# Kernel optimization log

Measured on AMD Instinct MI355X. Metric: run time of the kernel, lower is better.

## Reference

```python
import jax, jax.numpy as jnp
import numpy as np

M_SQRT1_2 = 0.7071067811865476
P_DROP = 0.1  # activation_dropout


def setup_inputs() -> dict:
    key = jax.random.key(0)
    k1, k2, k3, k4 = jax.random.split(key, 4)
    N, FFN, EMB = 8192, 4096, 1024
    x = jax.random.normal(k1, (N, FFN), dtype=jnp.float16)
    weight = (jax.random.normal(k2, (EMB, FFN), dtype=jnp.float32) * (1.0 / np.sqrt(FFN))).astype(jnp.float16)
    bias = jax.random.normal(k3, (EMB,), dtype=jnp.float16)
    mask = jax.random.uniform(k4, (N, FFN)) >= P_DROP  # keep mask (bool)
    return {"x": x, "weight": weight, "bias": bias, "mask": mask}


def reference(x, weight, bias, mask):
    # GELU computed in fp32, cast back to fp16 (matches the custom IR)
    xf = x.astype(jnp.float32)
    g = (0.5 * xf * (1.0 + jax.lax.erf(xf * M_SQRT1_2))).astype(jnp.float16)
    # dropout: mask then scale by 1/(1-p) in fp16
    scale = jnp.float16(1.0 / (1.0 - P_DROP))
    h = g * mask.astype(jnp.float16) * scale  # [N, FFN]
    # y[N0, N2] = sum_N1 h[N0, N1] * weight[N2, N1] + bias[N2]
    y = jnp.einsum('nf,ef->ne', h, weight) + bias[None, :]
    return y
```

## Files before the change

### kernel.cpp

```cpp
#include <hip/hip_runtime.h>
#include <stdint.h>

typedef uint32_t u32;
typedef uint16_t u16;

static constexpr int M_DIM = 8192;
static constexpr int N_DIM = 1024;
static constexpr int K_DIM = 4096;

static constexpr size_t H_BYTES  = (size_t)M_DIM * K_DIM * 2;
static constexpr size_t FRAG_U16 = 512;
static constexpr size_t WT_BYTES = 64ull * 128 * FRAG_U16 * 2;
static constexpr size_t WS_NEEDED = H_BYTES + WT_BYTES;

typedef __attribute__((ext_vector_type(8))) _Float16 half8;
typedef __attribute__((ext_vector_type(4))) float f32x4;

__device__ __forceinline__ u32 pack2(float a, float b) {
  union { _Float16 h[2]; u32 u; } p;
  p.h[0] = (_Float16)a;
  p.h[1] = (_Float16)b;
  return p.u;
}

__device__ __forceinline__ float gelu_drop(float x, u32 keep) {
  float ax = fabsf(x);
  float z  = ax * 0.70710678f;
  float t  = __builtin_amdgcn_rcpf(fmaf(0.3275911f, z, 1.0f));
  float poly = fmaf(fmaf(fmaf(fmaf(1.061405429f, t, -1.453152027f),
                              t, 1.421413741f),
                         t, -0.284496736f),
                    t, 0.254829592f) * t;
  float e   = exp2f(z * z * -1.44269504f);
  float erf = fmaf(-poly, e, 1.0f);
  float g   = 0.5f * x * (1.0f + copysignf(erf, x));
  return keep ? g * 1.1111112f : 0.0f;
}

__device__ __forceinline__ void async_cp16(const void* g, void* l) {
  __builtin_amdgcn_global_load_lds((__attribute__((address_space(1))) u32*)g,
                                   (__attribute__((address_space(3))) u32*)l,
                                   16, 0, 0);
}

static constexpr int W_PAIRS = 64 * 64;
static constexpr int WPACK_BLOCKS = W_PAIRS / 4;
static constexpr int PACKX_BLOCKS = 2048;
static constexpr u32 PACK_THREADS = PACKX_BLOCKS * 256;
static constexpr u32 PACK_GRANULES = (u32)((size_t)M_DIM * K_DIM / 4);
static constexpr int PACK_SWEEPS = PACK_GRANULES / PACK_THREADS;

__global__ __launch_bounds__(256)
void pack_kernel(const float* __restrict__ X, const int* __restrict__ Mask,
                 const float* __restrict__ W, u16* __restrict__ H, u16* __restrict__ Wt) {
  if (blockIdx.x < WPACK_BLOCKS) {
    const int l     = threadIdx.x & 63;
    const int pj    = blockIdx.x * 4 + (threadIdx.x >> 6);
    const int row16 = l & 15;
    const int kof   = (l >> 4) << 4;
    const int fsub  = kof >> 5;
    const int q0    = (kof & 31) >> 3;
    const int nb = pj >> 6, kp = pj & 63;
    const float* wp = W + (size_t)(nb * 16 + row16) * K_DIM + kp * 64 + kof;
    float4 w0 = *(const float4*)(wp + 0);
    float4 w1 = *(const float4*)(wp + 4);
    float4 w2 = *(const float4*)(wp + 8);
    float4 w3 = *(const float4*)(wp + 12);
    const int f = kp * 2 + fsub;
    u16* dst = Wt + (size_t)(nb * 128 + f) * FRAG_U16 + (size_t)(row16 + 16 * q0) * 8;
    *(uint4*)(dst)       = make_uint4(pack2(w0.x, w0.y), pack2(w0.z, w0.w),
                                      pack2(w1.x, w1.y), pack2(w1.z, w1.w));
    *(uint4*)(dst + 128) = make_uint4(pack2(w2.x, w2.y), pack2(w2.z, w2.w),
                                      pack2(w3.x, w3.y), pack2(w3.z, w3.w));
    return;
  }

  const u32 t0 = (blockIdx.x - WPACK_BLOCKS) * 256 + threadIdx.x;
  const float4* Xv = (const float4*)X;
  const uint4*  Mv = (const uint4*)Mask;

  u32 i = t0;
  float4 xA = Xv[i];
  uint4  mA = Mv[i];
  float4 xB;
  uint4  mB;

#pragma unroll
  for (int it = 0; it < PACK_SWEEPS; ++it) {
    const u32 inext = i + PACK_THREADS;
    if (it + 1 < PACK_SWEEPS) {
      xB = Xv[inext];
      mB = Mv[inext];
    }
    const u32 lo = pack2(gelu_drop(xA.x, mA.x), gelu_drop(xA.y, mA.y));
    const u32 hi = pack2(gelu_drop(xA.z, mA.z), gelu_drop(xA.w, mA.w));
    *(uint2*)(H + (size_t)i * 4) = make_uint2(lo, hi);
    i = inext;
    xA = xB;
    mA = mB;
  }
}

__global__ __launch_bounds__(256, 2)
void gemm_kernel(const u16* __restrict__ H, const u16* __restrict__ Wt,
                 const float* __restrict__ Bias, float* __restrict__ Out) {
  __shared__ __attribute__((aligned(16))) u16 Asl[2][8192];
  __shared__ __attribute__((aligned(16))) u16 Bsl[2][8192];

  const int tid  = threadIdx.x;
  const int lane = tid & 63;
  const int wv   = tid >> 6;
  const int wr   = wv >> 1;
  const int wc   = wv & 1;

  const int x  = blockIdx.x & 7;
  const int j  = blockIdx.x >> 3;
  const int bm = x * 8 + (j & 7);
  const int bn = j >> 3;
  const int m0 = bm * 128;
  const int n0 = bn * 128;

  const char* Hc = (const char*)H;
  const char* Wc = (const char*)Wt;

  size_t aSrc[4], bSrc[4];
#pragma unroll
  for (int p = 0; p < 4; ++p) {
    const int s = tid + 256 * p;
    const int row = s >> 3, ch = s & 7;
    aSrc[p] = (size_t)(m0 + row) * (K_DIM * 2) + (size_t)(((u32)ch ^ ((u32)row & 7u)) * 16);
    const int f = s >> 6;
    bSrc[p] = ((size_t)((bn * 8 + (f >> 1)) * 128 + (f & 1))) * 1024 + (size_t)(s & 63) * 16;
  }

  auto stage = [&](int ks, int buf) {
    const size_t ka = (size_t)ks * 128;
    const size_t kb = (size_t)ks * 2048;
#pragma unroll
    for (int p = 0; p < 4; ++p)
      async_cp16(Hc + aSrc[p] + ka, (char*)Asl[buf] + (size_t)(tid + 256 * p) * 16);
#pragma unroll
    for (int p = 0; p < 4; ++p)
      async_cp16(Wc + bSrc[p] + kb, (char*)Bsl[buf] + (size_t)(tid + 256 * p) * 16);
  };

  f32x4 acc[4][4];
#pragma unroll
  for (int i = 0; i < 4; ++i)
#pragma unroll
    for (int jj = 0; jj < 4; ++jj)
      acc[i][jj] = (f32x4){0.f, 0.f, 0.f, 0.f};

  stage(0, 0);
  __syncthreads();

  int buf = 0;
#pragma unroll 1
  for (int ks = 0; ks < 64; ++ks) {
    if (ks + 1 < 64) stage(ks + 1, buf ^ 1);

    const char* ac = (const char*)Asl[buf];
    const char* bc = (const char*)Bsl[buf];
#pragma unroll
    for (int kk = 0; kk < 2; ++kk) {
      half8 ar[4], br[4];
#pragma unroll
      for (int i = 0; i < 4; ++i) {
        const int row = wr * 64 + i * 16 + (lane & 15);
        const u32 ch = ((u32)(kk * 4 + (lane >> 4))) ^ ((u32)lane & 7u);
        ar[i] = *(const half8*)(ac + (size_t)row * 128 + ch * 16);
      }
#pragma unroll
      for (int jj = 0; jj < 4; ++jj)
        br[jj] = *(const half8*)(bc + (size_t)(((wc * 4 + jj) * 2 + kk) * 1024) + lane * 16);
#pragma unroll
      for (int i = 0; i < 4; ++i)
#pragma unroll
        for (int jj = 0; jj < 4; ++jj)
          acc[i][jj] = __builtin_amdgcn_mfma_f32_16x16x32_f16(ar[i], br[jj], acc[i][jj], 0, 0, 0);
    }
    __syncthreads();
    buf ^= 1;
  }

  const int fr = lane & 15;
  const int rq = (lane >> 4) << 2;
  float bv[4];
#pragma unroll
  for (int jj = 0; jj < 4; ++jj)
    bv[jj] = Bias[n0 + wc * 64 + jj * 16 + fr];
#pragma unroll
  for (int i = 0; i < 4; ++i) {
    const int row0 = m0 + wr * 64 + i * 16 + rq;
#pragma unroll
    for (int jj = 0; jj < 4; ++jj) {
      const int col = n0 + wc * 64 + jj * 16 + fr;
#pragma unroll
      for (int r = 0; r < 4; ++r)
        Out[(size_t)(row0 + r) * N_DIM + col] = acc[i][jj][r] + bv[jj];
    }
  }
}

static constexpr int A_STRIDE = 40;

__global__ __launch_bounds__(256, 2)
void fused_fallback_kernel(const float* __restrict__ X, const float* __restrict__ W,
                           const float* __restrict__ Bias, const int* __restrict__ Mask,
                           float* __restrict__ Out) {
  __shared__ __attribute__((aligned(16))) _Float16 As[128 * A_STRIDE];
  __shared__ __attribute__((aligned(16))) _Float16 Bs[128 * 32];

  const int tid  = threadIdx.x;
  const int lane = tid & 63;
  const int wv   = tid >> 6;
  const int wr   = wv >> 1;
  const int wc   = wv & 1;
  const int bm = blockIdx.x & 63;
  const int bn = blockIdx.x >> 6;
  const int m0 = bm * 128;
  const int n0 = bn * 128;

  const int a_m = tid >> 1;
  const int a_k = (tid & 1) << 4;
  const float* xptr = X    + (size_t)(m0 + a_m) * K_DIM + a_k;
  const int*   mptr = Mask + (size_t)(m0 + a_m) * K_DIM + a_k;
  _Float16* a_lds = &As[a_m * A_STRIDE + a_k];

  const int i0 = tid, i1 = tid + 256;
  const float* wp0 = W + (size_t)(n0 + (i0 >> 2)) * K_DIM + ((i0 & 3) << 3);
  const float* wp1 = W + (size_t)(n0 + (i1 >> 2)) * K_DIM + ((i1 & 3) << 3);
  _Float16* bl0 = &Bs[i0 * 8];
  _Float16* bl1 = &Bs[i1 * 8];

  f32x4 acc[4][4];
#pragma unroll
  for (int i = 0; i < 4; ++i)
#pragma unroll
    for (int j = 0; j < 4; ++j)
      acc[i][j] = (f32x4){0.f, 0.f, 0.f, 0.f};

  float4 xf0 = *(const float4*)(xptr +  0);
  float4 xf1 = *(const float4*)(xptr +  4);
  float4 xf2 = *(const float4*)(xptr +  8);
  float4 xf3 = *(const float4*)(xptr + 12);
  uint4  mr0 = *(const uint4*)(mptr +  0);
  uint4  mr1 = *(const uint4*)(mptr +  4);
  uint4  mr2 = *(const uint4*)(mptr +  8);
  uint4  mr3 = *(const uint4*)(mptr + 12);
  float4 wf0 = *(const float4*)(wp0 + 0);
  float4 wf1 = *(const float4*)(wp0 + 4);
  float4 wf2 = *(const float4*)(wp1 + 0);
  float4 wf3 = *(const float4*)(wp1 + 4);

#pragma unroll 1
  for (int kt = 0; kt < 128; ++kt) {
    {
      float xs[16] = {xf0.x, xf0.y, xf0.z, xf0.w, xf1.x, xf1.y, xf1.z, xf1.w,
                      xf2.x, xf2.y, xf2.z, xf2.w, xf3.x, xf3.y, xf3.z, xf3.w};
      u32 mk[16]   = {mr0.x, mr0.y, mr0.z, mr0.w, mr1.x, mr1.y, mr1.z, mr1.w,
                      mr2.x, mr2.y, mr2.z, mr2.w, mr3.x, mr3.y, mr3.z, mr3.w};
      u32 ow[8];
#pragma unroll
      for (int e = 0; e < 8; ++e)
        ow[e] = pack2(gelu_drop(xs[2 * e], mk[2 * e]), gelu_drop(xs[2 * e + 1], mk[2 * e + 1]));
      ((uint4*)a_lds)[0] = make_uint4(ow[0], ow[1], ow[2], ow[3]);
      ((uint4*)a_lds)[1] = make_uint4(ow[4], ow[5], ow[6], ow[7]);
    }
    {
      *(uint4*)bl0 = make_uint4(pack2(wf0.x, wf0.y), pack2(wf0.z, wf0.w),
                                pack2(wf1.x, wf1.y), pack2(wf1.z, wf1.w));
      *(uint4*)bl1 = make_uint4(pack2(wf2.x, wf2.y), pack2(wf2.z, wf2.w),
                                pack2(wf3.x, wf3.y), pack2(wf3.z, wf3.w));
    }
    __syncthreads();

    if (kt + 1 < 128) {
      xptr += 32; mptr += 32; wp0 += 32; wp1 += 32;
      xf0 = *(const float4*)(xptr +  0);
      xf1 = *(const float4*)(xptr +  4);
      xf2 = *(const float4*)(xptr +  8);
      xf3 = *(const float4*)(xptr + 12);
      mr0 = *(const uint4*)(mptr +  0);
      mr1 = *(const uint4*)(mptr +  4);
      mr2 = *(const uint4*)(mptr +  8);
      mr3 = *(const uint4*)(mptr + 12);
      wf0 = *(const float4*)(wp0 + 0);
      wf1 = *(const float4*)(wp0 + 4);
      wf2 = *(const float4*)(wp1 + 0);
      wf3 = *(const float4*)(wp1 + 4);
    }

    {
      const int fr2 = lane & 15;
      const int fk2 = (lane >> 4) << 3;
      half8 ar[4], br[4];
#pragma unroll
      for (int i = 0; i < 4; ++i)
        ar[i] = *(const half8*)&As[(wr * 64 + i * 16 + fr2) * A_STRIDE + fk2];
#pragma unroll
      for (int j = 0; j < 4; ++j)
        br[j] = *(const half8*)&Bs[(wc * 64 + j * 16 + fr2) * 32 + fk2];
#pragma unroll
      for (int i = 0; i < 4; ++i)
#pragma unroll
        for (int j = 0; j < 4; ++j)
          acc[i][j] = __builtin_amdgcn_mfma_f32_16x16x32_f16(ar[i], br[j], acc[i][j], 0, 0, 0);
    }
    __syncthreads();
  }

  const int fr = lane & 15;
  const int rq = (lane >> 4) << 2;
  float bv[4];
#pragma unroll
  for (int j = 0; j < 4; ++j)
    bv[j] = Bias[n0 + wc * 64 + j * 16 + fr];
#pragma unroll
  for (int i = 0; i < 4; ++i) {
    const int row0 = m0 + wr * 64 + i * 16 + rq;
#pragma unroll
    for (int j = 0; j < 4; ++j) {
      const int col = n0 + wc * 64 + j * 16 + fr;
#pragma unroll
      for (int r = 0; r < 4; ++r)
        Out[(size_t)(row0 + r) * N_DIM + col] = acc[i][j][r] + bv[j];
    }
  }
}

extern "C" void kernel_launch(void* const* d_in, const int* in_sizes, int n_in,
                              void* d_out, int out_size, void* d_ws, size_t ws_size,
                              hipStream_t stream) {
  const float* X    = (const float*)d_in[0];
  const float* W    = (const float*)d_in[1];
  const float* Bias = (const float*)d_in[2];
  const int*   Mk   = (const int*)d_in[3];
  float* Out = (float*)d_out;

  if (ws_size >= WS_NEEDED) {
    u16* H  = (u16*)d_ws;
    u16* Wt = (u16*)((char*)d_ws + H_BYTES);
    pack_kernel<<<WPACK_BLOCKS + PACKX_BLOCKS, 256, 0, stream>>>(X, Mk, W, H, Wt);
    gemm_kernel<<<(M_DIM / 128) * (N_DIM / 128), 256, 0, stream>>>(H, Wt, Bias, Out);
  } else {
    fused_fallback_kernel<<<64 * 8, 256, 0, stream>>>(X, W, Bias, Mk, Out);
  }
}
```

Baseline: 391.0 us.

## Stage pack-kernel X and mask loads through LDS with a 4-slot async pipeline

Replaces the grid-strided, register double-buffered GELU/dropout pack loop with block-contiguous chunks. Each chunk's X and mask are fetched with async global-to-LDS copies into a 4-slot ring, three chunks ahead. Explicit vmcnt waits, counted to include the outstanding H stores, gate each chunk before it is consumed. The aim is to keep more memory requests in flight and improve locality in this bandwidth-bound pre-pass. The cost is 32 KB of shared memory per block, which can reduce occupancy, including for the weight-pack blocks that never use it, and correctness depends on fragile hand-tuned waitcnt values.

```diff
diff --git a/kernel.cpp b/kernel.cpp
--- a/kernel.cpp
+++ b/kernel.cpp
@@ -46,13 +46,13 @@
 static constexpr int W_PAIRS = 64 * 64;
 static constexpr int WPACK_BLOCKS = W_PAIRS / 4;
 static constexpr int PACKX_BLOCKS = 2048;
-static constexpr u32 PACK_THREADS = PACKX_BLOCKS * 256;
-static constexpr u32 PACK_GRANULES = (u32)((size_t)M_DIM * K_DIM / 4);
-static constexpr int PACK_SWEEPS = PACK_GRANULES / PACK_THREADS;
+static constexpr int PACK_CHUNKS = 16;
 
 __global__ __launch_bounds__(256)
 void pack_kernel(const float* __restrict__ X, const int* __restrict__ Mask,
                  const float* __restrict__ W, u16* __restrict__ H, u16* __restrict__ Wt) {
+  __shared__ __attribute__((aligned(16))) char S[4][8192];
+
   if (blockIdx.x < WPACK_BLOCKS) {
     const int l     = threadIdx.x & 63;
     const int pj    = blockIdx.x * 4 + (threadIdx.x >> 6);
@@ -75,29 +75,43 @@
     return;
   }
 
-  const u32 t0 = (blockIdx.x - WPACK_BLOCKS) * 256 + threadIdx.x;
+  const int tid = threadIdx.x;
+  const size_t blockG = (size_t)(blockIdx.x - WPACK_BLOCKS) * (PACK_CHUNKS * 256);
   const float4* Xv = (const float4*)X;
   const uint4*  Mv = (const uint4*)Mask;
 
-  u32 i = t0;
-  float4 xA = Xv[i];
-  uint4  mA = Mv[i];
-  float4 xB;
-  uint4  mB;
-
-#pragma unroll
-  for (int it = 0; it < PACK_SWEEPS; ++it) {
-    const u32 inext = i + PACK_THREADS;
-    if (it + 1 < PACK_SWEEPS) {
-      xB = Xv[inext];
-      mB = Mv[inext];
-    }
-    const u32 lo = pack2(gelu_drop(xA.x, mA.x), gelu_drop(xA.y, mA.y));
-    const u32 hi = pack2(gelu_drop(xA.z, mA.z), gelu_drop(xA.w, mA.w));
-    *(uint2*)(H + (size_t)i * 4) = make_uint2(lo, hi);
-    i = inext;
-    xA = xB;
-    mA = mB;
+  auto stage = [&](int c) {
+    const int slot = c & 3;
+    const size_t g = blockG + (size_t)c * 256 + tid;
+    async_cp16(Xv + g, (char*)S + slot * 8192 + tid * 16);
+    async_cp16(Mv + g, (char*)S + slot * 8192 + 4096 + tid * 16);
+  };
+
+  stage(0);
+  stage(1);
+  stage(2);
+
+#pragma unroll
+  for (int c = 0; c < PACK_CHUNKS; ++c) {
+    if (c + 3 < PACK_CHUNKS) stage(c + 3);
+    const int nv = (c < 1) ? 6 : (c < 2) ? 7 : (c < 3) ? 8
+                 : (c < 13) ? 9 : (c == 13) ? 7 : (c == 14) ? 5 : 3;
+    switch (nv) {
+      case 3: asm volatile("s_waitcnt vmcnt(3)" ::: "memory"); break;
+      case 5: asm volatile("s_waitcnt vmcnt(5)" ::: "memory"); break;
+      case 6: asm volatile("s_waitcnt vmcnt(6)" ::: "memory"); break;
+      case 7: asm volatile("s_waitcnt vmcnt(7)" ::: "memory"); break;
+      case 8: asm volatile("s_waitcnt vmcnt(8)" ::: "memory"); break;
+      default: asm volatile("s_waitcnt vmcnt(9)" ::: "memory"); break;
+    }
+    __builtin_amdgcn_sched_barrier(0);
+    const int slot = c & 3;
+    const char* sb = (const char*)S + slot * 8192;
+    float4 xv = *(const float4*)(sb + tid * 16);
+    uint4  mv = *(const uint4*)(sb + 4096 + tid * 16);
+    const u32 lo = pack2(gelu_drop(xv.x, mv.x), gelu_drop(xv.y, mv.y));
+    const u32 hi = pack2(gelu_drop(xv.z, mv.z), gelu_drop(xv.w, mv.w));
+    *(uint2*)(H + (blockG + (size_t)c * 256 + tid) * 4) = make_uint2(lo, hi);
   }
 }
 
```

Result: no change. 397.6 us (+1.7%).
